# Kernel optimization log

Hardware: AMD Instinct MI355X
Metric: run time of the kernel (lower is better)

The kernel has to match this reference:

```python
import jax, jax.numpy as jnp
import numpy as np

N_RAYS = 32768
N_SAMPLES = N_RAYS * 32  # 1,048,576
FDIM = 32
HID = 64
RGB_HID = 64
THRESHOLD = 1e-4  # early_termination_threshold


def setup_inputs() -> dict:
    key = jax.random.key(0)
    ks = jax.random.split(key, 12)
    # ragged per-ray sample counts (avg 32), adjusted so total is exactly N_SAMPLES
    rng = np.random.default_rng(0)
    counts = rng.integers(8, 57, size=N_RAYS)
    delta = int(N_SAMPLES - counts.sum())
    if delta >= 0:
        counts[:delta] += 1
    else:
        counts[:(-delta)] -= 1
    starts = np.concatenate([[0], np.cumsum(counts)[:-1]])
    packing_info = jnp.asarray(np.stack([starts, counts], axis=1), dtype=jnp.int32)
    ray_ids = jnp.asarray(np.repeat(np.arange(N_RAYS), counts), dtype=jnp.int32)

    pos = jax.random.uniform(ks[0], (N_SAMPLES, 3), minval=-1.0, maxval=1.0)
    dirs = jax.random.normal(ks[1], (N_SAMPLES, 3))
    dirs = dirs / jnp.linalg.norm(dirs, axis=1, keepdims=True)
    dt = jax.random.uniform(ks[2], (N_SAMPLES, 1), minval=0.0, maxval=0.01)
    packed_samples = jnp.concatenate([pos, dirs, dt], axis=1)

    def lin(k, fi, fo):
        return jax.random.normal(k, (fi, fo)) / np.sqrt(fi)

    return {
        "packed_samples": packed_samples,
        "packing_info": packing_info,
        "ray_ids": ray_ids,
        "w1": lin(ks[3], 3, HID), "b1": jnp.zeros(HID),
        "w2": lin(ks[4], HID, FDIM), "b2": jnp.zeros(FDIM),
        "w_sigma": lin(ks[5], FDIM, 1), "b_sigma": jnp.zeros(1),
        "w_rgb1": lin(ks[6], FDIM + 3, RGB_HID), "b_rgb1": jnp.zeros(RGB_HID),
        "w_rgb2": lin(ks[7], RGB_HID, 3), "b_rgb2": jnp.zeros(3),
        "bg_color": jnp.ones(3),
    }


def reference(packed_samples, packing_info, ray_ids, w1, b1, w2, b2,
              w_sigma, b_sigma, w_rgb1, b_rgb1, w_rgb2, b_rgb2, bg_color):
    pos = packed_samples[:, :3]
    dirs = packed_samples[:, 3:6]
    dt = packed_samples[:, 6]

    # feature_module
    feats = jax.nn.relu(pos @ w1 + b1) @ w2 + b2            # [N, FDIM]
    # sigma_decoder
    sigma = jax.nn.softplus(feats @ w_sigma + b_sigma)[:, 0]  # [N]

    # NerfWeights: per-ray transmittance T_i = exp(-sum_{j<i in ray} sigma_j*dt_j),
    # weight_i = T_i * (1 - exp(-sigma_i*dt_i)), zeroed once T drops below threshold.
    tau = sigma * dt
    c_excl = jnp.cumsum(tau) - tau                           # exclusive global cumsum
    seg_base = c_excl[packing_info[:, 0]]                    # cumsum before each ray's start
    T = jnp.exp(-(c_excl - seg_base[ray_ids]))
    alpha = 1.0 - jnp.exp(-tau)
    weights = jnp.where(T > THRESHOLD, T * alpha, 0.0)       # [N]

    # rgb_decoder (masked gather in torch is a perf trick; weight==0 kills masked rgbs)
    h = jax.nn.relu(jnp.concatenate([feats, dirs], axis=1) @ w_rgb1 + b_rgb1)
    rgbs = jax.nn.sigmoid(h @ w_rgb2 + b_rgb2)               # [N, 3]

    contrib = rgbs * weights[:, None]
    rendered = jax.ops.segment_sum(contrib, ray_ids, num_segments=N_RAYS)   # [n_rays,3]
    opac = jax.ops.segment_sum(weights, ray_ids, num_segments=N_RAYS)       # [n_rays]
    return rendered + bg_color * (1.0 - opac[:, None])
```

## Files before the change

kernel.cpp:

```cpp
#include <hip/hip_runtime.h>
#include <hip/hip_bf16.h>
#include <math.h>
#include <stdint.h>

#define N_RAYS    32768
#define N_SAMPLES (N_RAYS * 32)
#define THRESH 0.0001f
#define TBL_OFF  (16u * 1024u * 1024u)

#define R_A1   0
#define R_A2   2
#define R_R1A  6
#define R_R1B  10
#define R_AR2  12
#define R_AR2F 16
#define R_B2I  18
#define R_ARI  22

typedef __attribute__((ext_vector_type(8)))  __bf16 bf16x8;
typedef __attribute__((ext_vector_type(16))) float  f32x16;
typedef float f4a __attribute__((ext_vector_type(4), aligned(4)));

union FragU  { __hip_bfloat162 h2[4]; uint32_t w[4]; bf16x8 v; };
union RecU   { bf16x8 v; uint4 u; };
union Rec16U { f32x16 v; uint4 u[4]; float f[16]; };

__device__ inline __hip_bfloat162 pk2(float lo, float hi) {
    float2 t; t.x = lo; t.y = hi;
    return __float22bfloat162_rn(t);
}

__device__ inline bf16x8 pack8(const float* vals) {
    FragU u;
    u.h2[0] = pk2(vals[0], vals[1]);
    u.h2[1] = pk2(vals[2], vals[3]);
    u.h2[2] = pk2(vals[4], vals[5]);
    u.h2[3] = pk2(vals[6], vals[7]);
    return u.v;
}

__device__ inline float rcp_fast(float x) {
    float r;
    asm("v_rcp_f32 %0, %1" : "=v"(r) : "v"(x));
    return r;
}
__device__ inline float sigmoid_fast(float x) { return rcp_fast(1.0f + __expf(-x)); }
__device__ inline float softplus_fast(float x) {
    const float e = __expf(-fabsf(x));
    return fmaxf(x, 0.0f) + __logf(1.0f + e);
}

template <int P>
__device__ inline bf16x8 packB_relu(f32x16 a) {
    FragU u;
    u.h2[0] = pk2(fmaxf(a[P+0],0.f), fmaxf(a[P+1],0.f));
    u.h2[1] = pk2(fmaxf(a[P+2],0.f), fmaxf(a[P+3],0.f));
    u.h2[2] = pk2(fmaxf(a[P+4],0.f), fmaxf(a[P+5],0.f));
    u.h2[3] = pk2(fmaxf(a[P+6],0.f), fmaxf(a[P+7],0.f));
    return u.v;
}
template <int P>
__device__ inline bf16x8 packB_plain(f32x16 a) {
    FragU u;
    u.h2[0] = pk2(a[P+0], a[P+1]);
    u.h2[1] = pk2(a[P+2], a[P+3]);
    u.h2[2] = pk2(a[P+4], a[P+5]);
    u.h2[3] = pk2(a[P+6], a[P+7]);
    return u.v;
}

__global__ __launch_bounds__(256) void nerf_build_frags(
    const float* __restrict__ w1,  const float* __restrict__ b1,
    const float* __restrict__ w2,  const float* __restrict__ b2,
    const float* __restrict__ w_sigma, const float* __restrict__ b_sigma,
    const float* __restrict__ w_rgb1,  const float* __restrict__ b_rgb1,
    const float* __restrict__ w_rgb2,  const float* __restrict__ b_rgb2,
    uint4* __restrict__ tbl)
{
    const int wid  = threadIdx.x >> 6;
    const int lane = threadIdx.x & 63;
    const int m    = lane & 31;
    const int h    = lane >> 5;
    RecU rec;

    if (wid == 0) {
        #pragma unroll
        for (int t = 0; t < 2; ++t) {
            float v[8] = {0,0,0,0,0,0,0,0};
            if (h == 0) {
                const int j = 32*t + m;
                v[0] = w1[j]; v[1] = w1[64+j]; v[2] = w1[128+j]; v[3] = b1[j];
            }
            rec.v = pack8(v); tbl[(R_A1+t)*64 + lane] = rec.u;
        }
        #pragma unroll
        for (int c = 0; c < 4; ++c) {
            float v[8];
            #pragma unroll
            for (int q = 0; q < 8; ++q) {
                const int j = 16*c + (q&3) + 8*(q>>2) + 4*h;
                v[q] = w2[j*32 + m];
            }
            rec.v = pack8(v); tbl[(R_A2+c)*64 + lane] = rec.u;
        }
    } else if (wid == 1) {
        #pragma unroll
        for (int t = 0; t < 2; ++t)
            #pragma unroll
            for (int c = 0; c < 2; ++c) {
                float v[8];
                #pragma unroll
                for (int q = 0; q < 8; ++q) {
                    const int f = 16*c + (q&3) + 8*(q>>2) + 4*h;
                    v[q] = w_rgb1[f*64 + 32*t + m];
                }
                rec.v = pack8(v); tbl[(R_R1A+2*t+c)*64 + lane] = rec.u;
            }
        #pragma unroll
        for (int t = 0; t < 2; ++t) {
            float v[8] = {0,0,0,0,0,0,0,0};
            if (h == 1) {
                const int j = 32*t + m;
                v[0] = w_rgb1[32*64 + j]; v[1] = w_rgb1[33*64 + j];
                v[2] = w_rgb1[34*64 + j]; v[3] = b_rgb1[j];
            }
            rec.v = pack8(v); tbl[(R_R1B+t)*64 + lane] = rec.u;
        }
    } else if (wid == 2) {
        #pragma unroll
        for (int c = 0; c < 4; ++c) {
            float v[8];
            #pragma unroll
            for (int q = 0; q < 8; ++q) {
                const int hh = 16*c + (q&3) + 8*(q>>2) + 4*h;
                v[q] = (m < 3) ? w_rgb2[hh*3 + m] : 0.0f;
            }
            rec.v = pack8(v); tbl[(R_AR2+c)*64 + lane] = rec.u;
        }
        #pragma unroll
        for (int c = 0; c < 2; ++c) {
            float v[8];
            #pragma unroll
            for (int q = 0; q < 8; ++q) {
                const int f = 16*c + (q&3) + 8*(q>>2) + 4*h;
                v[q] = (m == 3) ? w_sigma[f] : 0.0f;
            }
            rec.v = pack8(v); tbl[(R_AR2F+c)*64 + lane] = rec.u;
        }
        Rec16U r16;
        #pragma unroll
        for (int i = 0; i < 4; ++i) {
            #pragma unroll
            for (int e = 0; e < 4; ++e) r16.f[4*i+e] = b2[e + 8*i + 4*h];
        }
        #pragma unroll
        for (int i = 0; i < 4; ++i) tbl[(R_B2I+i)*64 + lane] = r16.u[i];
        #pragma unroll
        for (int i = 0; i < 4; ++i) {
            #pragma unroll
            for (int e = 0; e < 4; ++e) {
                const int r = e + 8*i + 4*h;
                r16.f[4*i+e] = (r < 3) ? b_rgb2[r] : ((r == 3) ? b_sigma[0] : 0.0f);
            }
        }
        #pragma unroll
        for (int i = 0; i < 4; ++i) tbl[(R_ARI+i)*64 + lane] = r16.u[i];
    }
}

__global__ __launch_bounds__(256, 2) void nerf_mlp_mfma(
    const float* __restrict__ samples,
    const uint4* __restrict__ tbl,
    float4* __restrict__ out)
{
    const int lane = threadIdx.x & 63;
    const int m32  = lane & 31;
    const int h    = lane >> 5;
    const int wgid = (blockIdx.x * blockDim.x + threadIdx.x) >> 6;
    const int base0 = wgid * 256;

    f4a sa[2], sb[2];
    {
        const float* sp = samples + (size_t)(base0 + m32) * 7;
        sa[0] = *(const f4a*)sp;  sb[0] = *(const f4a*)(sp + 3);
    }

    bf16x8 A1[2], A2[4], R1a[4], R1b[2], Ar2[4], Ar2f[2];
    f32x16 b2i, arinit;
    {
        RecU r_;
        #pragma unroll
        for (int t = 0; t < 2; ++t) { r_.u = tbl[(R_A1+t)*64 + lane];  A1[t]  = r_.v; }
        #pragma unroll
        for (int c = 0; c < 4; ++c) { r_.u = tbl[(R_A2+c)*64 + lane];  A2[c]  = r_.v; }
        #pragma unroll
        for (int i = 0; i < 4; ++i) { r_.u = tbl[(R_R1A+i)*64 + lane]; R1a[i] = r_.v; }
        #pragma unroll
        for (int t = 0; t < 2; ++t) { r_.u = tbl[(R_R1B+t)*64 + lane]; R1b[t] = r_.v; }
        #pragma unroll
        for (int c = 0; c < 4; ++c) { r_.u = tbl[(R_AR2+c)*64 + lane]; Ar2[c] = r_.v; }
        #pragma unroll
        for (int c = 0; c < 2; ++c) { r_.u = tbl[(R_AR2F+c)*64 + lane]; Ar2f[c] = r_.v; }
        Rec16U r16;
        #pragma unroll
        for (int i = 0; i < 4; ++i) r16.u[i] = tbl[(R_B2I+i)*64 + lane];
        b2i = r16.v;
        #pragma unroll
        for (int i = 0; i < 4; ++i) r16.u[i] = tbl[(R_ARI+i)*64 + lane];
        arinit = r16.v;
    }

    const f32x16 zero16 = {0,0,0,0,0,0,0,0,0,0,0,0,0,0,0,0};

    #pragma unroll
    for (int it = 0; it < 8; ++it) {
        const int cb = it & 1;
        const int nb = (it + 1) & 1;
        if (it < 7) {
            const float* sp = samples + (size_t)(base0 + (it + 1) * 32 + m32) * 7;
            sa[nb] = *(const f4a*)sp;  sb[nb] = *(const f4a*)(sp + 3);
        }

        FragU bin;
        bin.h2[0] = pk2(h ? sb[cb].x : sa[cb].x, h ? sb[cb].y : sa[cb].y);
        bin.h2[1] = pk2(h ? sb[cb].z : sa[cb].z, 1.0f);
        bin.w[2] = 0; bin.w[3] = 0;

        f32x16 accL1[2];
        #pragma unroll
        for (int t = 0; t < 2; ++t)
            accL1[t] = __builtin_amdgcn_mfma_f32_32x32x16_bf16(A1[t], bin.v, zero16, 0,0,0);

        bf16x8 B2c[4];
        B2c[0] = packB_relu<0>(accL1[0]);
        B2c[1] = packB_relu<8>(accL1[0]);
        B2c[2] = packB_relu<0>(accL1[1]);
        B2c[3] = packB_relu<8>(accL1[1]);

        f32x16 accL2;
        accL2 = __builtin_amdgcn_mfma_f32_32x32x16_bf16(A2[0], B2c[0], b2i, 0,0,0);
        accL2 = __builtin_amdgcn_mfma_f32_32x32x16_bf16(A2[1], B2c[1], accL2, 0,0,0);
        accL2 = __builtin_amdgcn_mfma_f32_32x32x16_bf16(A2[2], B2c[2], accL2, 0,0,0);
        accL2 = __builtin_amdgcn_mfma_f32_32x32x16_bf16(A2[3], B2c[3], accL2, 0,0,0);

        bf16x8 Bf[2];
        Bf[0] = packB_plain<0>(accL2);
        Bf[1] = packB_plain<8>(accL2);

        f32x16 ah[2];
        #pragma unroll
        for (int t = 0; t < 2; ++t) {
            ah[t] = __builtin_amdgcn_mfma_f32_32x32x16_bf16(R1a[2*t+0], Bf[0], zero16, 0,0,0);
            ah[t] = __builtin_amdgcn_mfma_f32_32x32x16_bf16(R1a[2*t+1], Bf[1], ah[t], 0,0,0);
            ah[t] = __builtin_amdgcn_mfma_f32_32x32x16_bf16(R1b[t],     bin.v, ah[t], 0,0,0);
        }

        bf16x8 Bh[4];
        Bh[0] = packB_relu<0>(ah[0]);
        Bh[1] = packB_relu<8>(ah[0]);
        Bh[2] = packB_relu<0>(ah[1]);
        Bh[3] = packB_relu<8>(ah[1]);

        f32x16 ar;
        ar = __builtin_amdgcn_mfma_f32_32x32x16_bf16(Ar2[0], Bh[0], arinit, 0,0,0);
        ar = __builtin_amdgcn_mfma_f32_32x32x16_bf16(Ar2[1], Bh[1], ar, 0,0,0);
        ar = __builtin_amdgcn_mfma_f32_32x32x16_bf16(Ar2[2], Bh[2], ar, 0,0,0);
        ar = __builtin_amdgcn_mfma_f32_32x32x16_bf16(Ar2[3], Bh[3], ar, 0,0,0);
        ar = __builtin_amdgcn_mfma_f32_32x32x16_bf16(Ar2f[0], Bf[0], ar, 0,0,0);
        ar = __builtin_amdgcn_mfma_f32_32x32x16_bf16(Ar2f[1], Bf[1], ar, 0,0,0);

        const float rr    = sigmoid_fast(ar[0]);
        const float gg    = sigmoid_fast(ar[1]);
        const float bb    = sigmoid_fast(ar[2]);
        const float sigma = softplus_fast(ar[3]);
        const float tau   = sigma * sb[cb].w;
        if (lane < 32) out[base0 + it * 32 + m32] = make_float4(tau, rr, gg, bb);
    }
}

__global__ __launch_bounds__(256) void nerf_render_kernel(
    const float4* __restrict__ smp,
    const int*    __restrict__ packing,
    const float*  __restrict__ bg,
    float*        __restrict__ out)
{
    const int gtid = blockIdx.x * blockDim.x + threadIdx.x;
    const int ray  = gtid >> 6;
    const int lane = threadIdx.x & 63;
    if (ray >= N_RAYS) return;

    const int start = packing[2 * ray];
    const int count = packing[2 * ray + 1];

    float tau = 0.0f, r = 0.0f, g = 0.0f, b = 0.0f;
    if (lane < count) {
        const float4 v = smp[start + lane];
        tau = v.x; r = v.y; g = v.z; b = v.w;
    }

    float incl = tau;
    #pragma unroll
    for (int off = 1; off < 64; off <<= 1) {
        const float v = __shfl_up(incl, off, 64);
        if (lane >= off) incl += v;
    }
    const float c_excl = incl - tau;

    const float T     = __expf(-c_excl);
    const float alpha = 1.0f - __expf(-tau);
    float w = (lane < count && T > THRESH) ? T * alpha : 0.0f;

    float cr = r * w, cg = g * w, cb = b * w;

    #pragma unroll
    for (int off = 32; off > 0; off >>= 1) {
        cr += __shfl_down(cr, off, 64);
        cg += __shfl_down(cg, off, 64);
        cb += __shfl_down(cb, off, 64);
        w  += __shfl_down(w,  off, 64);
    }

    if (lane == 0) {
        out[ray * 3 + 0] = cr + bg[0] * (1.0f - w);
        out[ray * 3 + 1] = cg + bg[1] * (1.0f - w);
        out[ray * 3 + 2] = cb + bg[2] * (1.0f - w);
    }
}

extern "C" void kernel_launch(void* const* d_in, const int* in_sizes, int n_in,
                              void* d_out, int out_size, void* d_ws, size_t ws_size,
                              hipStream_t stream) {
    const float* samples  = (const float*)d_in[0];
    const int*   packing  = (const int*)  d_in[1];
    const float* w1       = (const float*)d_in[3];
    const float* b1       = (const float*)d_in[4];
    const float* w2       = (const float*)d_in[5];
    const float* b2       = (const float*)d_in[6];
    const float* w_sigma  = (const float*)d_in[7];
    const float* b_sigma  = (const float*)d_in[8];
    const float* w_rgb1   = (const float*)d_in[9];
    const float* b_rgb1   = (const float*)d_in[10];
    const float* w_rgb2   = (const float*)d_in[11];
    const float* b_rgb2   = (const float*)d_in[12];
    const float* bg       = (const float*)d_in[13];

    float4* smp = (float4*)d_ws;
    uint4*  tbl = (uint4*)((char*)d_ws + TBL_OFF);
    float*  out = (float*)d_out;

    nerf_build_frags<<<1, 256, 0, stream>>>(
        w1, b1, w2, b2, w_sigma, b_sigma,
        w_rgb1, b_rgb1, w_rgb2, b_rgb2, tbl);

    nerf_mlp_mfma<<<1024, 256, 0, stream>>>(samples, tbl, (float4*)smp);

    nerf_render_kernel<<<(N_RAYS * 64) / 256, 256, 0, stream>>>(smp, packing, bg, out);
}
```

Baseline: 47.54 us.

## Stage MLP weight fragments in LDS and raise occupancy to three blocks

Weight fragments are no longer held in registers for the whole kernel. Each block copies the weight table into shared memory once, and each MFMA reads its A operand from LDS on demand. Launch bounds go from 2 to 3 blocks per CU to take advantage of the freed registers and hide latency. In exchange it adds LDS reads in the inner loop, a block-wide barrier, and about 26 KB of LDS per block, which may itself cap occupancy.

```diff
diff --git a/kernel.cpp b/kernel.cpp
--- a/kernel.cpp
+++ b/kernel.cpp
@@ -16,6 +16,7 @@
 #define R_AR2F 16
 #define R_B2I  18
 #define R_ARI  22
+#define NREC   26
 
 typedef __attribute__((ext_vector_type(8)))  __bf16 bf16x8;
 typedef __attribute__((ext_vector_type(16))) float  f32x16;
@@ -168,11 +169,15 @@
     }
 }
 
-__global__ __launch_bounds__(256, 2) void nerf_mlp_mfma(
+__global__ __launch_bounds__(256, 3) void nerf_mlp_mfma(
     const float* __restrict__ samples,
     const uint4* __restrict__ tbl,
     float4* __restrict__ out)
 {
+    __shared__ uint4 wlds[NREC * 64];
+
+    for (int i = threadIdx.x; i < NREC * 64; i += 256) wlds[i] = tbl[i];
+
     const int lane = threadIdx.x & 63;
     const int m32  = lane & 31;
     const int h    = lane >> 5;
@@ -185,22 +190,8 @@
         sa[0] = *(const f4a*)sp;  sb[0] = *(const f4a*)(sp + 3);
     }
 
-    bf16x8 A1[2], A2[4], R1a[4], R1b[2], Ar2[4], Ar2f[2];
     f32x16 b2i, arinit;
     {
-        RecU r_;
-        #pragma unroll
-        for (int t = 0; t < 2; ++t) { r_.u = tbl[(R_A1+t)*64 + lane];  A1[t]  = r_.v; }
-        #pragma unroll
-        for (int c = 0; c < 4; ++c) { r_.u = tbl[(R_A2+c)*64 + lane];  A2[c]  = r_.v; }
-        #pragma unroll
-        for (int i = 0; i < 4; ++i) { r_.u = tbl[(R_R1A+i)*64 + lane]; R1a[i] = r_.v; }
-        #pragma unroll
-        for (int t = 0; t < 2; ++t) { r_.u = tbl[(R_R1B+t)*64 + lane]; R1b[t] = r_.v; }
-        #pragma unroll
-        for (int c = 0; c < 4; ++c) { r_.u = tbl[(R_AR2+c)*64 + lane]; Ar2[c] = r_.v; }
-        #pragma unroll
-        for (int c = 0; c < 2; ++c) { r_.u = tbl[(R_AR2F+c)*64 + lane]; Ar2f[c] = r_.v; }
         Rec16U r16;
         #pragma unroll
         for (int i = 0; i < 4; ++i) r16.u[i] = tbl[(R_B2I+i)*64 + lane];
@@ -209,6 +200,11 @@
         for (int i = 0; i < 4; ++i) r16.u[i] = tbl[(R_ARI+i)*64 + lane];
         arinit = r16.v;
     }
+
+    __syncthreads();
+
+    const uint4* wl = &wlds[lane];
+    #define LDW(rec) ({ RecU r_; r_.u = wl[(rec)*64]; r_.v; })
 
     const f32x16 zero16 = {0,0,0,0,0,0,0,0,0,0,0,0,0,0,0,0};
 
@@ -226,48 +222,42 @@
         bin.h2[1] = pk2(h ? sb[cb].z : sa[cb].z, 1.0f);
         bin.w[2] = 0; bin.w[3] = 0;
 
-        f32x16 accL1[2];
-        #pragma unroll
-        for (int t = 0; t < 2; ++t)
-            accL1[t] = __builtin_amdgcn_mfma_f32_32x32x16_bf16(A1[t], bin.v, zero16, 0,0,0);
-
         bf16x8 B2c[4];
-        B2c[0] = packB_relu<0>(accL1[0]);
-        B2c[1] = packB_relu<8>(accL1[0]);
-        B2c[2] = packB_relu<0>(accL1[1]);
-        B2c[3] = packB_relu<8>(accL1[1]);
-
-        f32x16 accL2;
-        accL2 = __builtin_amdgcn_mfma_f32_32x32x16_bf16(A2[0], B2c[0], b2i, 0,0,0);
-        accL2 = __builtin_amdgcn_mfma_f32_32x32x16_bf16(A2[1], B2c[1], accL2, 0,0,0);
-        accL2 = __builtin_amdgcn_mfma_f32_32x32x16_bf16(A2[2], B2c[2], accL2, 0,0,0);
-        accL2 = __builtin_amdgcn_mfma_f32_32x32x16_bf16(A2[3], B2c[3], accL2, 0,0,0);
-
-        bf16x8 Bf[2];
-        Bf[0] = packB_plain<0>(accL2);
-        Bf[1] = packB_plain<8>(accL2);
-
-        f32x16 ah[2];
+        {
+            f32x16 a0 = __builtin_amdgcn_mfma_f32_32x32x16_bf16(LDW(R_A1+0), bin.v, zero16, 0,0,0);
+            B2c[0] = packB_relu<0>(a0);
+            B2c[1] = packB_relu<8>(a0);
+            f32x16 a1 = __builtin_amdgcn_mfma_f32_32x32x16_bf16(LDW(R_A1+1), bin.v, zero16, 0,0,0);
+            B2c[2] = packB_relu<0>(a1);
+            B2c[3] = packB_relu<8>(a1);
+        }
+
+        f32x16 acc2;
+        acc2 = __builtin_amdgcn_mfma_f32_32x32x16_bf16(LDW(R_A2+0), B2c[0], b2i, 0,0,0);
+        acc2 = __builtin_amdgcn_mfma_f32_32x32x16_bf16(LDW(R_A2+1), B2c[1], acc2, 0,0,0);
+        acc2 = __builtin_amdgcn_mfma_f32_32x32x16_bf16(LDW(R_A2+2), B2c[2], acc2, 0,0,0);
+        acc2 = __builtin_amdgcn_mfma_f32_32x32x16_bf16(LDW(R_A2+3), B2c[3], acc2, 0,0,0);
+        bf16x8 Bf0 = packB_plain<0>(acc2);
+        bf16x8 Bf1 = packB_plain<8>(acc2);
+
+        bf16x8 Bh[4];
         #pragma unroll
         for (int t = 0; t < 2; ++t) {
-            ah[t] = __builtin_amdgcn_mfma_f32_32x32x16_bf16(R1a[2*t+0], Bf[0], zero16, 0,0,0);
-            ah[t] = __builtin_amdgcn_mfma_f32_32x32x16_bf16(R1a[2*t+1], Bf[1], ah[t], 0,0,0);
-            ah[t] = __builtin_amdgcn_mfma_f32_32x32x16_bf16(R1b[t],     bin.v, ah[t], 0,0,0);
-        }
-
-        bf16x8 Bh[4];
-        Bh[0] = packB_relu<0>(ah[0]);
-        Bh[1] = packB_relu<8>(ah[0]);
-        Bh[2] = packB_relu<0>(ah[1]);
-        Bh[3] = packB_relu<8>(ah[1]);
+            f32x16 a;
+            a = __builtin_amdgcn_mfma_f32_32x32x16_bf16(LDW(R_R1A+2*t+0), Bf0, zero16, 0,0,0);
+            a = __builtin_amdgcn_mfma_f32_32x32x16_bf16(LDW(R_R1A+2*t+1), Bf1, a, 0,0,0);
+            a = __builtin_amdgcn_mfma_f32_32x32x16_bf16(LDW(R_R1B+t),     bin.v, a, 0,0,0);
+            Bh[2*t+0] = packB_relu<0>(a);
+            Bh[2*t+1] = packB_relu<8>(a);
+        }
 
         f32x16 ar;
-        ar = __builtin_amdgcn_mfma_f32_32x32x16_bf16(Ar2[0], Bh[0], arinit, 0,0,0);
-        ar = __builtin_amdgcn_mfma_f32_32x32x16_bf16(Ar2[1], Bh[1], ar, 0,0,0);
-        ar = __builtin_amdgcn_mfma_f32_32x32x16_bf16(Ar2[2], Bh[2], ar, 0,0,0);
-        ar = __builtin_amdgcn_mfma_f32_32x32x16_bf16(Ar2[3], Bh[3], ar, 0,0,0);
-        ar = __builtin_amdgcn_mfma_f32_32x32x16_bf16(Ar2f[0], Bf[0], ar, 0,0,0);
-        ar = __builtin_amdgcn_mfma_f32_32x32x16_bf16(Ar2f[1], Bf[1], ar, 0,0,0);
+        ar = __builtin_amdgcn_mfma_f32_32x32x16_bf16(LDW(R_AR2+0), Bh[0], arinit, 0,0,0);
+        ar = __builtin_amdgcn_mfma_f32_32x32x16_bf16(LDW(R_AR2+1), Bh[1], ar, 0,0,0);
+        ar = __builtin_amdgcn_mfma_f32_32x32x16_bf16(LDW(R_AR2+2), Bh[2], ar, 0,0,0);
+        ar = __builtin_amdgcn_mfma_f32_32x32x16_bf16(LDW(R_AR2+3), Bh[3], ar, 0,0,0);
+        ar = __builtin_amdgcn_mfma_f32_32x32x16_bf16(LDW(R_AR2F+0), Bf0, ar, 0,0,0);
+        ar = __builtin_amdgcn_mfma_f32_32x32x16_bf16(LDW(R_AR2F+1), Bf1, ar, 0,0,0);
 
         const float rr    = sigmoid_fast(ar[0]);
         const float gg    = sigmoid_fast(ar[1]);
@@ -276,6 +266,7 @@
         const float tau   = sigma * sb[cb].w;
         if (lane < 32) out[base0 + it * 32 + m32] = make_float4(tau, rr, gg, bb);
     }
+    #undef LDW
 }
 
 __global__ __launch_bounds__(256) void nerf_render_kernel(
```

After: 48.56 us. 1.02x slower.
